# Optimization experiments

Hardware: AMD Instinct MI355X
Metric: run time of the kernel (lower is better)

The kernel has to match this reference:

```python
import jax, jax.numpy as jnp
import numpy as np

C = 2048
EPS = 1e-12


def conv1x1(x, w, b):
    # x: [B,C_in,H,W], w: [C_out,C_in], b: [C_out]
    return jnp.einsum('oc,bchw->bohw', w, x) + b[None, :, None, None]


def unfold3x3(x):
    # torch F.unfold(kernel=3, padding=1): output [B, C*9, H*W],
    # feature order (c, ki, kj) with c slowest.
    B, Cc, H, W = x.shape
    xp = jnp.pad(x, ((0, 0), (0, 0), (1, 1), (1, 1)))
    patches = jnp.stack([xp[:, :, ki:ki + H, kj:kj + W]
                         for ki in range(3) for kj in range(3)], axis=2)  # [B,C,9,H,W]
    return patches.reshape(B, Cc * 9, H * W)


def fold3x3(u, H, W):
    # torch F.fold(kernel=3, padding=1): overlap-add. u: [B, C*9, H*W]
    B = u.shape[0]
    Cc = u.shape[1] // 9
    t = u.reshape(B, Cc, 3, 3, H, W)
    out = jnp.zeros((B, Cc, H + 2, W + 2), dtype=u.dtype)
    for ki in range(3):
        for kj in range(3):
            out = out.at[:, :, ki:ki + H, kj:kj + W].add(t[:, :, ki, kj])
    return out[:, :, 1:1 + H, 1:1 + W]


def l2norm(x, axis):
    n = jnp.sqrt(jnp.sum(x * x, axis=axis, keepdims=True))
    return x / jnp.maximum(n, EPS)


def setup_inputs() -> dict:
    key = jax.random.key(0)
    ks = jax.random.split(key, 8)
    B, H, W = 4, 24, 24
    s = 0.02
    return {
        'part_ref': jax.random.normal(ks[0], (B, C, H, W), jnp.float32),
        'part_target': jax.random.normal(ks[1], (B, C, H, W), jnp.float32),
        'wq': jax.random.normal(ks[2], (C, C), jnp.float32) * s,
        'bq': jnp.zeros((C,), jnp.float32),
        'wk': jax.random.normal(ks[3], (C, C), jnp.float32) * s,
        'bk': jnp.zeros((C,), jnp.float32),
        'wt': jax.random.normal(ks[4], (C, 2 * C), jnp.float32) * s,
        'bt': jnp.zeros((C,), jnp.float32),
    }


def reference(part_ref, part_target, wq, bq, wk, bk, wt, bt):
    B, _, H, W = part_ref.shape
    part_target_o = part_target
    k = conv1x1(part_ref, wk, bk)
    q = conv1x1(part_target, wq, bq)

    tgt_unf = unfold3x3(q)        # [B, C*9, L]
    ref_unf1 = unfold3x3(k)       # [B, C*9, L]

    ref_n = l2norm(jnp.transpose(ref_unf1, (0, 2, 1)), axis=2)  # [B, L, C*9]
    tgt_n = l2norm(tgt_unf, axis=1)                              # [B, C*9, L]

    R = jnp.einsum('blc,bcm->blm', ref_n, tgt_n)  # [B, L_ref, L_tgt]
    R_star = jnp.max(R, axis=1)                   # [B, L]
    R_arg = jnp.argmax(R, axis=1)                 # [B, L]

    # gather best ref patch per target location along dim 2
    T_unf = jnp.take_along_axis(ref_unf1, R_arg[:, None, :], axis=2)  # [B, C*9, L]
    T_part = fold3x3(T_unf, H, W) / 9.0

    S = R_star.reshape(B, 1, H, W)
    x_res = jnp.concatenate((q, T_part), axis=1)  # [B, 2C, H, W]
    res = conv1x1(x_res, wt, bt) * S + part_target_o
    return res
```

## Files before the change

### kernel.cpp

```cpp
#include <hip/hip_runtime.h>
#include <cstddef>
#include <cstdint>

#define LPIX 576
#define CCH  2048
#define NB   4

typedef __attribute__((ext_vector_type(8))) short short8;
typedef __attribute__((ext_vector_type(4))) float f32x4;
typedef __attribute__((ext_vector_type(16))) float f32x16;
typedef __attribute__((ext_vector_type(4))) unsigned short u16x4;

__device__ __forceinline__ unsigned short f2bf(float f) {
    uint32_t u = __builtin_bit_cast(uint32_t, f);
    u += 0x7fff + ((u >> 16) & 1);
    return (unsigned short)(u >> 16);
}
__device__ __forceinline__ float bf2f(unsigned short s) {
    return __builtin_bit_cast(float, (uint32_t)s << 16);
}

__device__ __forceinline__ void gload_lds16(const void* g, void* l) {
    __builtin_amdgcn_global_load_lds((const __attribute__((address_space(1))) void*)g,
                                     (__attribute__((address_space(3))) void*)l, 16, 0, 0);
}

template<int BM, int BN>
__device__ __forceinline__ void mm32_core(
    const short* __restrict__ Ab, int lda,
    const short* __restrict__ Bb, int ldb,
    int k0, int kend, short* As, short* Bs,
    int m0, int n0, f32x16 (&acc)[BM / 32][BN / 64])
{
    constexpr int T   = 128;
    constexpr int NA  = BM * 8 / T;
    constexpr int NBC = BN * 8 / T;
    constexpr int ABUF = BM * 64;
    constexpr int BBUF = BN * 64;

    const int tid  = threadIdx.x;
    const int lane = tid & 63;
    const int w    = tid >> 6;
    const int wn   = w * (BN / 2);
    const int u31  = lane & 31;
    const int h    = lane >> 5;

    const short* Aptr[NA]; short* Alds[NA];
    #pragma unroll
    for (int t = 0; t < NA; ++t) {
        const int c   = t * T + tid;
        const int p   = c / (BM * 4);
        const int cip = c % (BM * 4);
        const int row = cip >> 2, q = cip & 3;
        const int s   = q ^ ((row >> 1) & 3);
        Aptr[t] = Ab + (size_t)(m0 + row) * lda + p * 32 + s * 8;
        Alds[t] = As + c * 8;
    }
    const short* Bptr[NBC]; short* Blds[NBC];
    #pragma unroll
    for (int t = 0; t < NBC; ++t) {
        const int c   = t * T + tid;
        const int p   = c / (BN * 4);
        const int cip = c % (BN * 4);
        const int row = cip >> 2, q = cip & 3;
        const int s   = q ^ ((row >> 1) & 3);
        Bptr[t] = Bb + (size_t)(n0 + row) * ldb + p * 32 + s * 8;
        Blds[t] = Bs + c * 8;
    }

    const int nsteps = (kend - k0) >> 6;

    #pragma unroll
    for (int t = 0; t < NA; ++t)  gload_lds16(Aptr[t] + k0, Alds[t]);
    #pragma unroll
    for (int t = 0; t < NBC; ++t) gload_lds16(Bptr[t] + k0, Blds[t]);
    __syncthreads();

    for (int it = 0; it < nsteps; ++it) {
        const int cur = it & 1;
        const short* Ac = As + cur * ABUF;
        const short* Bc = Bs + cur * BBUF;
        if (it + 1 < nsteps) {
            const int c1 = k0 + (it + 1) * 64;
            const int nb = cur ^ 1;
            #pragma unroll
            for (int t = 0; t < NA; ++t)  gload_lds16(Aptr[t] + c1, Alds[t] + nb * ABUF);
            #pragma unroll
            for (int t = 0; t < NBC; ++t) gload_lds16(Bptr[t] + c1, Blds[t] + nb * BBUF);
        }
        #pragma unroll
        for (int t4 = 0; t4 < 4; ++t4) {
            const int p = t4 >> 1;
            const int s = (t4 & 1) * 2 + h;
            short8 fa[BM / 32], fb[BN / 64];
            #pragma unroll
            for (int i = 0; i < BM / 32; ++i) {
                const int row = i * 32 + u31;
                fa[i] = *(const short8*)(Ac + p * BM * 32 + row * 32 + ((s ^ ((row >> 1) & 3)) * 8));
            }
            #pragma unroll
            for (int j = 0; j < BN / 64; ++j) {
                const int row = wn + j * 32 + u31;
                fb[j] = *(const short8*)(Bc + p * BN * 32 + row * 32 + ((s ^ ((row >> 1) & 3)) * 8));
            }
            #pragma unroll
            for (int i = 0; i < BM / 32; ++i)
                #pragma unroll
                for (int j = 0; j < BN / 64; ++j)
                    acc[i][j] = __builtin_amdgcn_mfma_f32_32x32x16_bf16(fa[i], fb[j], acc[i][j], 0, 0, 0);
        }
        __syncthreads();
    }
}

#define ROW32(r, h) (((r) & 3) + 8 * ((r) >> 2) + 4 * (h))

__global__ __launch_bounds__(256) void wcast2_k(const float* __restrict__ wq,
                                                const float* __restrict__ wk,
                                                short* __restrict__ Wb) {
    const float* W = blockIdx.y ? wk : wq;
    short* D = Wb + (size_t)blockIdx.y * CCH * CCH;
    int i = (blockIdx.x * 256 + threadIdx.x) * 4;
    float4 v = *(const float4*)(W + i);
    u16x4 u;
    u.x = f2bf(v.x); u.y = f2bf(v.y); u.z = f2bf(v.z); u.w = f2bf(v.w);
    *(u16x4*)(D + i) = u;
}

__global__ __launch_bounds__(256) void wcast_k(const float* __restrict__ W,
                                               short* __restrict__ Wb) {
    int i = (blockIdx.x * 256 + threadIdx.x) * 4;
    float4 v = *(const float4*)(W + i);
    u16x4 u;
    u.x = f2bf(v.x); u.y = f2bf(v.y); u.z = f2bf(v.z); u.w = f2bf(v.w);
    *(u16x4*)(Wb + i) = u;
}

__global__ __launch_bounds__(256) void tcast_k(const float* __restrict__ tgt,
                                               const float* __restrict__ ref,
                                               short* __restrict__ T1) {
    __shared__ float tile[32][33];
    const int z = blockIdx.z;
    const int b = z & 3, which = z >> 2;
    const float* X = (which ? ref : tgt) + (size_t)b * CCH * LPIX;
    const int c0 = blockIdx.y * 32;
    const int l0 = blockIdx.x * 32;
    const int tx = threadIdx.x, ty = threadIdx.y;
    #pragma unroll
    for (int j = 0; j < 4; ++j)
        tile[ty + j * 8][tx] = X[(size_t)(c0 + ty + j * 8) * LPIX + l0 + tx];
    __syncthreads();
    short* D = T1 + ((size_t)(which * NB + b) * LPIX) * CCH;
    #pragma unroll
    for (int j = 0; j < 4; ++j)
        D[(size_t)(l0 + ty + j * 8) * CCH + c0 + tx] = (short)f2bf(tile[tx][ty + j * 8]);
}

__global__ __launch_bounds__(128) void conv_k(
    const short* __restrict__ T1, const short* __restrict__ Wb,
    const float* __restrict__ bq, const float* __restrict__ bk,
    short* __restrict__ x2t, short* __restrict__ kt,
    float* __restrict__ nq, float* __restrict__ nk)
{
    __shared__ short As[2 * 64 * 64];
    __shared__ short Bs[2 * 128 * 64];
    const int id = blockIdx.x;
    const int xcd = id & 7, slot = id >> 3;
    const int sid = xcd * 4 + slot / 36;
    const int r36 = slot % 36;
    const int which = sid >> 4;
    const int m0 = (r36 % 9) * 64;
    const int n0 = (sid & 15) * 128;
    const int b  = r36 / 9;
    const short* Ab = T1 + (size_t)(which * NB + b) * LPIX * CCH;
    const short* Bb = Wb + (size_t)which * CCH * CCH;
    const float* bias = which ? bk : bq;
    short* Yb = which ? (kt + (size_t)b * LPIX * CCH) : (x2t + (size_t)b * LPIX * 4096);
    float* Nb = (which ? nk : nq) + b * LPIX;
    const int ldy = which ? CCH : 4096;

    f32x16 acc[2][2] = {};
    mm32_core<64, 128>(Ab, CCH, Bb, CCH, 0, CCH, As, Bs, m0, n0, acc);

    const int lane = threadIdx.x & 63, w = threadIdx.x >> 6;
    const int wn = w * 64, u31 = lane & 31, h = lane >> 5;
    #pragma unroll
    for (int i = 0; i < 2; ++i) {
        float pv[16];
        #pragma unroll
        for (int r = 0; r < 16; ++r) pv[r] = 0.f;
        #pragma unroll
        for (int j = 0; j < 2; ++j) {
            const int gn = n0 + wn + j * 32 + u31;
            const float bi = bias[gn];
            #pragma unroll
            for (int r = 0; r < 16; ++r) {
                const int gm = m0 + i * 32 + ROW32(r, h);
                float v = acc[i][j][r] + bi;
                pv[r] += v * v;
                Yb[(size_t)gm * ldy + gn] = (short)f2bf(v);
            }
        }
        #pragma unroll
        for (int r = 0; r < 16; ++r) {
            float s = pv[r];
            #pragma unroll
            for (int m = 1; m < 32; m <<= 1) s += __shfl_xor(s, m);
            if (u31 == 0) {
                const int gm = m0 + i * 32 + ROW32(r, h);
                atomicAdd(&Nb[gm], s);
            }
        }
    }
}

__global__ __launch_bounds__(128) void gram_k(
    const short* __restrict__ kt, const short* __restrict__ x2t,
    float* __restrict__ Mpart)
{
    __shared__ short As[2 * 64 * 64];
    __shared__ short Bs[2 * 64 * 64];
    const int z = blockIdx.z;
    const int b = z >> 1, kc = z & 1;
    const short* Ab = kt + (size_t)b * LPIX * CCH;
    const short* Bb = x2t + (size_t)b * LPIX * 4096;
    const int m0 = blockIdx.y * 64;
    const int n0 = blockIdx.x * 64;
    f32x16 acc[2][1] = {};
    mm32_core<64, 64>(Ab, CCH, Bb, 4096, kc * 1024, kc * 1024 + 1024, As, Bs, m0, n0, acc);
    float* Mb = Mpart + (size_t)(kc * NB + b) * LPIX * LPIX;
    const int lane = threadIdx.x & 63, w = threadIdx.x >> 6;
    const int wn = w * 32, u31 = lane & 31, h = lane >> 5;
    #pragma unroll
    for (int i = 0; i < 2; ++i) {
        const int gn = n0 + wn + u31;
        #pragma unroll
        for (int r = 0; r < 16; ++r) {
            const int gm = m0 + i * 32 + ROW32(r, h);
            Mb[(size_t)gm * LPIX + gn] = acc[i][0][r];
        }
    }
}

__global__ __launch_bounds__(128) void fin_k(
    const short* __restrict__ wtb, const short* __restrict__ x2t,
    const float* __restrict__ bt, const float* __restrict__ S,
    const float* __restrict__ PT, float* __restrict__ out)
{
    __shared__ short As[2 * 64 * 64];
    __shared__ short Bs[2 * 128 * 64];
    const int id = blockIdx.x;
    const int xcd = id & 7, slot = id >> 3;
    const int sid = xcd * 4 + slot / 18;
    const int m0 = sid * 64;
    const int n0 = (slot % 18) * 128;
    f32x16 acc[2][2] = {};
    mm32_core<64, 128>(wtb, 4096, x2t, 4096, 0, 4096, As, Bs, m0, n0, acc);
    const int lane = threadIdx.x & 63, w = threadIdx.x >> 6;
    const int wn = w * 64, u31 = lane & 31, h = lane >> 5;
    #pragma unroll
    for (int i = 0; i < 2; ++i)
        #pragma unroll
        for (int j = 0; j < 2; ++j) {
            const int gn = n0 + wn + j * 32 + u31;
            const int bb = gn / LPIX;
            const int l  = gn - bb * LPIX;
            const float sv = S[gn];
            #pragma unroll
            for (int r = 0; r < 16; ++r) {
                const int gm = m0 + i * 32 + ROW32(r, h);
                float v = (acc[i][j][r] + bt[gm]) * sv
                        + PT[((size_t)bb * CCH + gm) * LPIX + l];
                out[((size_t)bb * CCH + gm) * LPIX + l] = v;
            }
        }
}

__global__ __launch_bounds__(256) void argmax1_k(
    const float* __restrict__ Mpart, const float* __restrict__ nk,
    float* __restrict__ Pv, int* __restrict__ Pi)
{
    const int b   = blockIdx.z;
    const int lrb = blockIdx.y;
    const int tx = threadIdx.x, ty = threadIdx.y;
    const int tid = ty * 64 + tx;
    __shared__ float invNkS[24];
    if (tid < 24) {
        const int jr = tid;
        float s = 0.f;
        #pragma unroll
        for (int di = -1; di <= 1; ++di) {
            const int ii = lrb + di;
            if ((unsigned)ii > 23u) continue;
            #pragma unroll
            for (int dj = -1; dj <= 1; ++dj) {
                const int jj = jr + dj;
                if ((unsigned)jj > 23u) continue;
                s += nk[b * LPIX + ii * 24 + jj];
            }
        }
        invNkS[jr] = 1.0f / fmaxf(sqrtf(s), 1e-12f);
    }
    __syncthreads();
    const int lt = blockIdx.x * 64 + tx;
    const int it = lt / 24, jt = lt % 24;
    const float* Mb0 = Mpart + (size_t)b * LPIX * LPIX;
    const float* Mb1 = Mpart + (size_t)(NB + b) * LPIX * LPIX;
    float best = -1e30f; int bidx = 0;
    #pragma unroll
    for (int i = 0; i < 6; ++i) {
        const int jr = ty + i * 4;
        const int lr = lrb * 24 + jr;
        const int base = lr * LPIX + lt;
        float g = 0.f;
        #pragma unroll
        for (int di = -1; di <= 1; ++di) {
            if ((unsigned)(lrb + di) > 23u || (unsigned)(it + di) > 23u) continue;
            #pragma unroll
            for (int dj = -1; dj <= 1; ++dj) {
                if ((unsigned)(jr + dj) > 23u || (unsigned)(jt + dj) > 23u) continue;
                const int o = base + (di * 24 + dj) * (LPIX + 1);
                g += Mb0[o] + Mb1[o];
            }
        }
        float v = g * invNkS[jr];
        if (v > best) { best = v; bidx = lr; }
    }
    __shared__ float rv[4][64];
    __shared__ int   ri[4][64];
    rv[ty][tx] = best; ri[ty][tx] = bidx;
    __syncthreads();
    if (ty == 0) {
        #pragma unroll
        for (int y = 1; y < 4; ++y) {
            float v = rv[y][tx]; int id = ri[y][tx];
            if (v > best || (v == best && id < bidx)) { best = v; bidx = id; }
        }
        Pv[((size_t)b * 24 + lrb) * LPIX + lt] = best;
        Pi[((size_t)b * 24 + lrb) * LPIX + lt] = bidx;
    }
}

__global__ __launch_bounds__(256) void argmax2_k(
    const float* __restrict__ Pv, const int* __restrict__ Pi,
    const float* __restrict__ nq,
    float* __restrict__ S, int* __restrict__ Arg)
{
    int idx = blockIdx.x * 256 + threadIdx.x;
    if (idx >= NB * LPIX) return;
    int b = idx / LPIX, lt = idx % LPIX;
    int it = lt / 24, jt = lt % 24;
    float s = 0.f;
    #pragma unroll
    for (int di = -1; di <= 1; ++di) {
        const int ii = it + di;
        if ((unsigned)ii > 23u) continue;
        #pragma unroll
        for (int dj = -1; dj <= 1; ++dj) {
            const int jj = jt + dj;
            if ((unsigned)jj > 23u) continue;
            s += nq[b * LPIX + ii * 24 + jj];
        }
    }
    const float invNq = 1.0f / fmaxf(sqrtf(s), 1e-12f);
    float best = -1e30f; int bidx = 0;
    #pragma unroll
    for (int c = 0; c < 24; ++c) {
        float v = Pv[((size_t)b * 24 + c) * LPIX + lt];
        int  id = Pi[((size_t)b * 24 + c) * LPIX + lt];
        if (v > best || (v == best && id < bidx)) { best = v; bidx = id; }
    }
    S[idx]   = best * invNq;
    Arg[idx] = bidx;
}

__global__ __launch_bounds__(256) void gather_k(
    const short* __restrict__ kt, const int* __restrict__ Arg,
    short* __restrict__ x2t)
{
    const int id = blockIdx.x;
    const int xcd = id & 7, slot = id >> 3;
    const int b  = xcd >> 1;
    const int l0 = ((xcd & 1) * 72 + slot) * 4;
    const int lane = threadIdx.x, ty = threadIdx.y;
    const int tid = ty * 64 + lane;
    __shared__ int tap[4][9];
    if (tid < 36) {
        int px = tid / 9, t9 = tid % 9;
        int l = l0 + px;
        int i = l / 24, j = l % 24;
        int ki = t9 / 3, kj = t9 % 3;
        int ip = i + 1 - ki, jp = j + 1 - kj;
        int off = -1;
        if (ip >= 0 && ip < 24 && jp >= 0 && jp < 24) {
            int a = Arg[b * LPIX + ip * 24 + jp];
            int rr = a / 24 + ki - 1;
            int cc = a % 24 + kj - 1;
            if (rr >= 0 && rr < 24 && cc >= 0 && cc < 24) off = rr * 24 + cc;
        }
        tap[px][t9] = off;
    }
    __syncthreads();
    const int l = l0 + ty;
    const short* Kb = kt + (size_t)b * LPIX * CCH;
    short* dst = x2t + ((size_t)b * LPIX + l) * 4096 + CCH;
    int t[9];
    #pragma unroll
    for (int i = 0; i < 9; ++i) t[i] = tap[ty][i];
    const float inv9 = 1.0f / 9.0f;
    #pragma unroll
    for (int j = 0; j < 8; ++j) {
        int c = (lane + j * 64) * 4;
        float s0 = 0.f, s1 = 0.f, s2 = 0.f, s3 = 0.f;
        #pragma unroll
        for (int t9 = 0; t9 < 9; ++t9) {
            int off = t[t9];
            if (off < 0) continue;
            u16x4 u = *(const u16x4*)(Kb + (size_t)off * CCH + c);
            s0 += bf2f(u.x); s1 += bf2f(u.y); s2 += bf2f(u.z); s3 += bf2f(u.w);
        }
        u16x4 o;
        o.x = f2bf(s0 * inv9); o.y = f2bf(s1 * inv9);
        o.z = f2bf(s2 * inv9); o.w = f2bf(s3 * inv9);
        *(u16x4*)(dst + c) = o;
    }
}

extern "C" void kernel_launch(void* const* d_in, const int* in_sizes, int n_in,
                              void* d_out, int out_size, void* d_ws, size_t ws_size,
                              hipStream_t stream) {
    const float* part_ref = (const float*)d_in[0];
    const float* part_tgt = (const float*)d_in[1];
    const float* wq = (const float*)d_in[2];
    const float* bq = (const float*)d_in[3];
    const float* wk = (const float*)d_in[4];
    const float* bk = (const float*)d_in[5];
    const float* wt = (const float*)d_in[6];
    const float* bt = (const float*)d_in[7];
    float* out = (float*)d_out;

    short* wqb2 = (short*)d_ws;
    short* wtb  = wqb2;
    short* T1   = wqb2 + (size_t)2 * CCH * CCH;
    short* kt   = T1 + (size_t)2 * NB * LPIX * CCH;
    short* x2t  = kt + (size_t)NB * LPIX * CCH;
    float* Mpart = (float*)T1;
    float* nk    = (float*)(x2t + (size_t)NB * LPIX * 4096);
    float* nq    = nk + NB * LPIX;
    float* Sbuf  = nq + NB * LPIX;
    int*   Arg   = (int*)(Sbuf + NB * LPIX);
    float* Pv    = (float*)(Arg + NB * LPIX);
    int*   Pi    = (int*)(Pv + (size_t)24 * NB * LPIX);

    hipMemsetAsync(nk, 0, 2 * NB * LPIX * sizeof(float), stream);

    wcast2_k<<<dim3(4096, 2), 256, 0, stream>>>(wq, wk, wqb2);
    tcast_k<<<dim3(18, 64, 8), dim3(32, 8), 0, stream>>>(part_tgt, part_ref, T1);

    conv_k<<<1152, 128, 0, stream>>>(T1, wqb2, bq, bk, x2t, kt, nq, nk);

    gram_k<<<dim3(9, 9, 8), 128, 0, stream>>>(kt, x2t, Mpart);

    argmax1_k<<<dim3(9, 24, NB), dim3(64, 4), 0, stream>>>(Mpart, nk, Pv, Pi);
    argmax2_k<<<9, 256, 0, stream>>>(Pv, Pi, nq, Sbuf, Arg);

    gather_k<<<576, dim3(64, 4), 0, stream>>>(kt, Arg, x2t);

    wcast_k<<<8192, 256, 0, stream>>>(wt, wtb);
    fin_k<<<576, 128, 0, stream>>>(wtb, x2t, bt, Sbuf, part_tgt, out);
}
```

Measured before the change: 411.2 us.

## Retile GEMM core to 256-thread 2x2 warps, single-buffer LDS, split-K final conv

Rewrites the shared MFMA GEMM core to use 256 threads arranged as a 2x2 wave grid over 128x128 tiles. It uses a single LDS buffer with an XOR-swizzled 64-wide row layout in place of the previous double-buffered prefetch. The conv kernel now covers all batches in one M dimension with larger tiles. The final conv is split along K into two halves that accumulate into a zeroed output via atomicAdd. This aims for more reuse per tile and better occupancy, but it gives up load/compute overlap and adds an output memset plus float atomics, which also make the summation order nondeterministic.

```diff
diff --git a/kernel.cpp b/kernel.cpp
--- a/kernel.cpp
+++ b/kernel.cpp
@@ -7,7 +7,6 @@
 #define NB   4
 
 typedef __attribute__((ext_vector_type(8))) short short8;
-typedef __attribute__((ext_vector_type(4))) float f32x4;
 typedef __attribute__((ext_vector_type(16))) float f32x16;
 typedef __attribute__((ext_vector_type(4))) unsigned short u16x4;
 
@@ -25,95 +24,70 @@
                                      (__attribute__((address_space(3))) void*)l, 16, 0, 0);
 }
 
-template<int BM, int BN>
+#define ROW32(r, h) (((r) & 3) + 8 * ((r) >> 2) + 4 * (h))
+
+template<int BM, int BN, int FM, int FN>
 __device__ __forceinline__ void mm32_core(
     const short* __restrict__ Ab, int lda,
     const short* __restrict__ Bb, int ldb,
     int k0, int kend, short* As, short* Bs,
-    int m0, int n0, f32x16 (&acc)[BM / 32][BN / 64])
-{
-    constexpr int T   = 128;
-    constexpr int NA  = BM * 8 / T;
-    constexpr int NBC = BN * 8 / T;
-    constexpr int ABUF = BM * 64;
-    constexpr int BBUF = BN * 64;
-
+    int m0, int n0, f32x16 (&acc)[FM][FN])
+{
+    constexpr int NA  = BM * 8 / 256;
+    constexpr int NBC = BN * 8 / 256;
     const int tid  = threadIdx.x;
     const int lane = tid & 63;
     const int w    = tid >> 6;
-    const int wn   = w * (BN / 2);
+    const int wr   = w & 1, wc = w >> 1;
     const int u31  = lane & 31;
     const int h    = lane >> 5;
 
     const short* Aptr[NA]; short* Alds[NA];
     #pragma unroll
     for (int t = 0; t < NA; ++t) {
-        const int c   = t * T + tid;
-        const int p   = c / (BM * 4);
-        const int cip = c % (BM * 4);
-        const int row = cip >> 2, q = cip & 3;
-        const int s   = q ^ ((row >> 1) & 3);
-        Aptr[t] = Ab + (size_t)(m0 + row) * lda + p * 32 + s * 8;
+        const int c = t * 256 + tid;
+        const int row = c >> 3, sl = c & 7;
+        Aptr[t] = Ab + (size_t)(m0 + row) * lda + ((sl ^ (row & 7)) * 8);
         Alds[t] = As + c * 8;
     }
     const short* Bptr[NBC]; short* Blds[NBC];
     #pragma unroll
     for (int t = 0; t < NBC; ++t) {
-        const int c   = t * T + tid;
-        const int p   = c / (BN * 4);
-        const int cip = c % (BN * 4);
-        const int row = cip >> 2, q = cip & 3;
-        const int s   = q ^ ((row >> 1) & 3);
-        Bptr[t] = Bb + (size_t)(n0 + row) * ldb + p * 32 + s * 8;
+        const int c = t * 256 + tid;
+        const int row = c >> 3, sl = c & 7;
+        Bptr[t] = Bb + (size_t)(n0 + row) * ldb + ((sl ^ (row & 7)) * 8);
         Blds[t] = Bs + c * 8;
     }
 
-    const int nsteps = (kend - k0) >> 6;
-
-    #pragma unroll
-    for (int t = 0; t < NA; ++t)  gload_lds16(Aptr[t] + k0, Alds[t]);
-    #pragma unroll
-    for (int t = 0; t < NBC; ++t) gload_lds16(Bptr[t] + k0, Blds[t]);
-    __syncthreads();
-
-    for (int it = 0; it < nsteps; ++it) {
-        const int cur = it & 1;
-        const short* Ac = As + cur * ABUF;
-        const short* Bc = Bs + cur * BBUF;
-        if (it + 1 < nsteps) {
-            const int c1 = k0 + (it + 1) * 64;
-            const int nb = cur ^ 1;
-            #pragma unroll
-            for (int t = 0; t < NA; ++t)  gload_lds16(Aptr[t] + c1, Alds[t] + nb * ABUF);
-            #pragma unroll
-            for (int t = 0; t < NBC; ++t) gload_lds16(Bptr[t] + c1, Blds[t] + nb * BBUF);
-        }
+    for (int c0 = k0; c0 < kend; c0 += 64) {
+        #pragma unroll
+        for (int t = 0; t < NA; ++t)  gload_lds16(Aptr[t] + c0, Alds[t]);
+        #pragma unroll
+        for (int t = 0; t < NBC; ++t) gload_lds16(Bptr[t] + c0, Blds[t]);
+        __syncthreads();
         #pragma unroll
         for (int t4 = 0; t4 < 4; ++t4) {
-            const int p = t4 >> 1;
-            const int s = (t4 & 1) * 2 + h;
-            short8 fa[BM / 32], fb[BN / 64];
-            #pragma unroll
-            for (int i = 0; i < BM / 32; ++i) {
-                const int row = i * 32 + u31;
-                fa[i] = *(const short8*)(Ac + p * BM * 32 + row * 32 + ((s ^ ((row >> 1) & 3)) * 8));
-            }
-            #pragma unroll
-            for (int j = 0; j < BN / 64; ++j) {
-                const int row = wn + j * 32 + u31;
-                fb[j] = *(const short8*)(Bc + p * BN * 32 + row * 32 + ((s ^ ((row >> 1) & 3)) * 8));
-            }
-            #pragma unroll
-            for (int i = 0; i < BM / 32; ++i)
+            const int g = 2 * t4 + h;
+            short8 fa[FM], fb[FN];
+            #pragma unroll
+            for (int i = 0; i < FM; ++i) {
+                const int row = wr * 32 * FM + i * 32 + u31;
+                fa[i] = *(const short8*)(As + row * 64 + ((g ^ (row & 7)) * 8));
+            }
+            #pragma unroll
+            for (int j = 0; j < FN; ++j) {
+                const int row = wc * 32 * FN + j * 32 + u31;
+                fb[j] = *(const short8*)(Bs + row * 64 + ((g ^ (row & 7)) * 8));
+            }
+            #pragma unroll
+            for (int i = 0; i < FM; ++i)
                 #pragma unroll
-                for (int j = 0; j < BN / 64; ++j)
+                for (int j = 0; j < FN; ++j)
                     acc[i][j] = __builtin_amdgcn_mfma_f32_32x32x16_bf16(fa[i], fb[j], acc[i][j], 0, 0, 0);
         }
         __syncthreads();
     }
 }
-
-#define ROW32(r, h) (((r) & 3) + 8 * ((r) >> 2) + 4 * (h))
 
 __global__ __launch_bounds__(256) void wcast2_k(const float* __restrict__ wq,
                                                 const float* __restrict__ wk,
@@ -156,34 +130,33 @@
         D[(size_t)(l0 + ty + j * 8) * CCH + c0 + tx] = (short)f2bf(tile[tx][ty + j * 8]);
 }
 
-__global__ __launch_bounds__(128) void conv_k(
+__global__ __launch_bounds__(256) void conv_k(
     const short* __restrict__ T1, const short* __restrict__ Wb,
     const float* __restrict__ bq, const float* __restrict__ bk,
     short* __restrict__ x2t, short* __restrict__ kt,
     float* __restrict__ nq, float* __restrict__ nk)
 {
-    __shared__ short As[2 * 64 * 64];
-    __shared__ short Bs[2 * 128 * 64];
+    __shared__ short As[128 * 64];
+    __shared__ short Bs[128 * 64];
     const int id = blockIdx.x;
     const int xcd = id & 7, slot = id >> 3;
-    const int sid = xcd * 4 + slot / 36;
-    const int r36 = slot % 36;
+    const int sid = xcd * 4 + slot / 18;
     const int which = sid >> 4;
-    const int m0 = (r36 % 9) * 64;
     const int n0 = (sid & 15) * 128;
-    const int b  = r36 / 9;
-    const short* Ab = T1 + (size_t)(which * NB + b) * LPIX * CCH;
+    const int m0 = (slot % 18) * 128;
+    const short* Ab = T1 + (size_t)which * (NB * LPIX) * CCH;
     const short* Bb = Wb + (size_t)which * CCH * CCH;
     const float* bias = which ? bk : bq;
-    short* Yb = which ? (kt + (size_t)b * LPIX * CCH) : (x2t + (size_t)b * LPIX * 4096);
-    float* Nb = (which ? nk : nq) + b * LPIX;
+    short* Yb = which ? kt : x2t;
     const int ldy = which ? CCH : 4096;
+    float* Narr = which ? nk : nq;
 
     f32x16 acc[2][2] = {};
-    mm32_core<64, 128>(Ab, CCH, Bb, CCH, 0, CCH, As, Bs, m0, n0, acc);
+    mm32_core<128, 128, 2, 2>(Ab, CCH, Bb, CCH, 0, CCH, As, Bs, m0, n0, acc);
 
     const int lane = threadIdx.x & 63, w = threadIdx.x >> 6;
-    const int wn = w * 64, u31 = lane & 31, h = lane >> 5;
+    const int wr = w & 1, wc = w >> 1;
+    const int u31 = lane & 31, h = lane >> 5;
     #pragma unroll
     for (int i = 0; i < 2; ++i) {
         float pv[16];
@@ -191,11 +164,11 @@
         for (int r = 0; r < 16; ++r) pv[r] = 0.f;
         #pragma unroll
         for (int j = 0; j < 2; ++j) {
-            const int gn = n0 + wn + j * 32 + u31;
+            const int gn = n0 + wc * 64 + j * 32 + u31;
             const float bi = bias[gn];
             #pragma unroll
             for (int r = 0; r < 16; ++r) {
-                const int gm = m0 + i * 32 + ROW32(r, h);
+                const int gm = m0 + wr * 64 + i * 32 + ROW32(r, h);
                 float v = acc[i][j][r] + bi;
                 pv[r] += v * v;
                 Yb[(size_t)gm * ldy + gn] = (short)f2bf(v);
@@ -207,71 +180,73 @@
             #pragma unroll
             for (int m = 1; m < 32; m <<= 1) s += __shfl_xor(s, m);
             if (u31 == 0) {
-                const int gm = m0 + i * 32 + ROW32(r, h);
-                atomicAdd(&Nb[gm], s);
-            }
-        }
-    }
-}
-
-__global__ __launch_bounds__(128) void gram_k(
+                const int gm = m0 + wr * 64 + i * 32 + ROW32(r, h);
+                atomicAdd(&Narr[gm], s);
+            }
+        }
+    }
+}
+
+__global__ __launch_bounds__(256) void gram_k(
     const short* __restrict__ kt, const short* __restrict__ x2t,
     float* __restrict__ Mpart)
 {
-    __shared__ short As[2 * 64 * 64];
-    __shared__ short Bs[2 * 64 * 64];
+    __shared__ short As[64 * 64];
+    __shared__ short Bs[64 * 64];
     const int z = blockIdx.z;
     const int b = z >> 1, kc = z & 1;
     const short* Ab = kt + (size_t)b * LPIX * CCH;
     const short* Bb = x2t + (size_t)b * LPIX * 4096;
     const int m0 = blockIdx.y * 64;
     const int n0 = blockIdx.x * 64;
-    f32x16 acc[2][1] = {};
-    mm32_core<64, 64>(Ab, CCH, Bb, 4096, kc * 1024, kc * 1024 + 1024, As, Bs, m0, n0, acc);
+    f32x16 acc[1][1] = {};
+    mm32_core<64, 64, 1, 1>(Ab, CCH, Bb, 4096, kc * 1024, kc * 1024 + 1024, As, Bs, m0, n0, acc);
     float* Mb = Mpart + (size_t)(kc * NB + b) * LPIX * LPIX;
     const int lane = threadIdx.x & 63, w = threadIdx.x >> 6;
-    const int wn = w * 32, u31 = lane & 31, h = lane >> 5;
-    #pragma unroll
-    for (int i = 0; i < 2; ++i) {
-        const int gn = n0 + wn + u31;
-        #pragma unroll
-        for (int r = 0; r < 16; ++r) {
-            const int gm = m0 + i * 32 + ROW32(r, h);
-            Mb[(size_t)gm * LPIX + gn] = acc[i][0][r];
-        }
-    }
-}
-
-__global__ __launch_bounds__(128) void fin_k(
+    const int wr = w & 1, wc = w >> 1;
+    const int u31 = lane & 31, h = lane >> 5;
+    const int gn = n0 + wc * 32 + u31;
+    #pragma unroll
+    for (int r = 0; r < 16; ++r) {
+        const int gm = m0 + wr * 32 + ROW32(r, h);
+        Mb[(size_t)gm * LPIX + gn] = acc[0][0][r];
+    }
+}
+
+__global__ __launch_bounds__(256) void fin_k(
     const short* __restrict__ wtb, const short* __restrict__ x2t,
     const float* __restrict__ bt, const float* __restrict__ S,
     const float* __restrict__ PT, float* __restrict__ out)
 {
-    __shared__ short As[2 * 64 * 64];
-    __shared__ short Bs[2 * 128 * 64];
+    __shared__ short As[128 * 64];
+    __shared__ short Bs[128 * 64];
     const int id = blockIdx.x;
     const int xcd = id & 7, slot = id >> 3;
     const int sid = xcd * 4 + slot / 18;
-    const int m0 = sid * 64;
+    const int kc = sid >> 4;
+    const int m0 = (sid & 15) * 128;
     const int n0 = (slot % 18) * 128;
     f32x16 acc[2][2] = {};
-    mm32_core<64, 128>(wtb, 4096, x2t, 4096, 0, 4096, As, Bs, m0, n0, acc);
+    mm32_core<128, 128, 2, 2>(wtb, 4096, x2t, 4096, kc * 2048, kc * 2048 + 2048,
+                              As, Bs, m0, n0, acc);
     const int lane = threadIdx.x & 63, w = threadIdx.x >> 6;
-    const int wn = w * 64, u31 = lane & 31, h = lane >> 5;
+    const int wr = w & 1, wc = w >> 1;
+    const int u31 = lane & 31, h = lane >> 5;
     #pragma unroll
     for (int i = 0; i < 2; ++i)
         #pragma unroll
         for (int j = 0; j < 2; ++j) {
-            const int gn = n0 + wn + j * 32 + u31;
+            const int gn = n0 + wc * 64 + j * 32 + u31;
             const int bb = gn / LPIX;
             const int l  = gn - bb * LPIX;
             const float sv = S[gn];
             #pragma unroll
             for (int r = 0; r < 16; ++r) {
-                const int gm = m0 + i * 32 + ROW32(r, h);
-                float v = (acc[i][j][r] + bt[gm]) * sv
-                        + PT[((size_t)bb * CCH + gm) * LPIX + l];
-                out[((size_t)bb * CCH + gm) * LPIX + l] = v;
+                const int gm = m0 + wr * 64 + i * 32 + ROW32(r, h);
+                const size_t idx = ((size_t)bb * CCH + gm) * LPIX + l;
+                float v = kc ? (acc[i][j][r] + bt[gm]) * sv + PT[idx]
+                             : acc[i][j][r] * sv;
+                atomicAdd(&out[idx], v);
             }
         }
 }
@@ -453,13 +428,14 @@
     int*   Pi    = (int*)(Pv + (size_t)24 * NB * LPIX);
 
     hipMemsetAsync(nk, 0, 2 * NB * LPIX * sizeof(float), stream);
+    hipMemsetAsync(out, 0, (size_t)NB * CCH * LPIX * sizeof(float), stream);
 
     wcast2_k<<<dim3(4096, 2), 256, 0, stream>>>(wq, wk, wqb2);
     tcast_k<<<dim3(18, 64, 8), dim3(32, 8), 0, stream>>>(part_tgt, part_ref, T1);
 
-    conv_k<<<1152, 128, 0, stream>>>(T1, wqb2, bq, bk, x2t, kt, nq, nk);
-
-    gram_k<<<dim3(9, 9, 8), 128, 0, stream>>>(kt, x2t, Mpart);
+    conv_k<<<576, 256, 0, stream>>>(T1, wqb2, bq, bk, x2t, kt, nq, nk);
+
+    gram_k<<<dim3(9, 9, 8), 256, 0, stream>>>(kt, x2t, Mpart);
 
     argmax1_k<<<dim3(9, 24, NB), dim3(64, 4), 0, stream>>>(Mpart, nk, Pv, Pi);
     argmax2_k<<<9, 256, 0, stream>>>(Pv, Pi, nq, Sbuf, Arg);
@@ -467,5 +443,5 @@
     gather_k<<<576, dim3(64, 4), 0, stream>>>(kt, Arg, x2t);
 
     wcast_k<<<8192, 256, 0, stream>>>(wt, wtb);
-    fin_k<<<576, 128, 0, stream>>>(wtb, x2t, bt, Sbuf, part_tgt, out);
-}
+    fin_k<<<576, 256, 0, stream>>>(wtb, x2t, bt, Sbuf, part_tgt, out);
+}
```

Result: faster. 394.1 us (-4.2%).
